# Kernel tuning notes

Hardware: AMD Instinct MI355X
Metric: run time of the kernel (lower is better)

## Reference

```python
import jax, jax.numpy as jnp
import numpy as np

# ---- ATSSPostProcessor config ----
PRE_NMS_THRESH = 0.05
PRE_NMS_TOP_N  = 400      # k candidates per image (pre_nms_top_n)
NMS_THRESH     = 0.4
POST_TOP_N     = 100      # fpn_post_nms_top_n
MIN_SIZE       = 0.0
NUM_ANGLE_BINS = 90
BBOX_W         = (10.0, 10.0, 5.0, 5.0)   # box_coder xywh weights; angle is passthrough (argmax-90 deg)
N, C, H, W     = 4, 15, 256, 256           # A=1 anchor per location
STRIDE, ANCHOR_SIZE = 8.0, 64.0
MAXV = 16                                   # vertex buffer for quad-quad clipping


def setup_inputs():
    key = jax.random.key(0)
    k1, k2, k3, k4 = jax.random.split(key, 4)
    box_cls = jax.random.normal(k1, (N, C, H, W), jnp.float32) - 2.0  # sigmoid ~0.12 avg -> plenty of candidates
    box_regression = jax.random.normal(k2, (N, 4, H, W), jnp.float32) * 0.5
    centerness = jax.random.normal(k3, (N, 1, H, W), jnp.float32)
    angle = jax.random.normal(k4, (N, NUM_ANGLE_BINS, H, W), jnp.float32)
    # xywha anchors on the stride-8 grid, row-major (H, W) to match permute_and_flatten ordering
    ys, xs = jnp.meshgrid(jnp.arange(H, dtype=jnp.float32), jnp.arange(W, dtype=jnp.float32), indexing='ij')
    cx = (xs.reshape(-1) + 0.5) * STRIDE
    cy = (ys.reshape(-1) + 0.5) * STRIDE
    wh = jnp.full((H * W,), ANCHOR_SIZE, jnp.float32)
    a0 = jnp.zeros((H * W,), jnp.float32)
    anchors = jnp.broadcast_to(jnp.stack([cx, cy, wh, wh, a0], -1), (N, H * W, 5))
    return {"box_cls": box_cls, "box_regression": box_regression, "centerness": centerness,
            "angle": angle, "anchors": jnp.asarray(anchors)}


def xywha_to_corners(b):
    # b [..., 5] (cx,cy,w,h,angle_deg) -> [..., 4, 2], CCW order
    cx, cy, w, h, a = b[..., 0], b[..., 1], b[..., 2], b[..., 3], b[..., 4]
    t = a * (jnp.pi / 180.0)
    c, s = jnp.cos(t), jnp.sin(t)
    ox = jnp.asarray([1., -1., -1., 1.], b.dtype) * (w[..., None] * 0.5)
    oy = jnp.asarray([1., 1., -1., -1.], b.dtype) * (h[..., None] * 0.5)
    x = cx[..., None] + ox * c[..., None] - oy * s[..., None]
    y = cy[..., None] + ox * s[..., None] + oy * c[..., None]
    return jnp.stack([x, y], -1)


def _clip_edge(poly, n, p1, p2):
    # Sutherland-Hodgman: clip CCW polygon (poly[:n]) against half-plane left of p1->p2
    e = p2 - p1
    d = e[0] * (poly[:, 1] - p1[1]) - e[1] * (poly[:, 0] - p1[0])  # >= 0 is inside
    def body(i, carry):
        out, m = carry
        j = jnp.where(i == n - 1, 0, i + 1)
        cur, nxt, dc, dn = poly[i], poly[j], d[i], d[j]
        denom = dc - dn
        denom = jnp.where(jnp.abs(denom) < 1e-8, 1e-8, denom)
        ip = cur + (dc / denom) * (nxt - cur)
        act = i < n
        a1 = act & (dc >= 0)
        out = out.at[m].set(jnp.where(a1, cur, out[m]))
        m = m + a1.astype(jnp.int32)
        a2 = act & ((dc >= 0) != (dn >= 0))
        out = out.at[m].set(jnp.where(a2, ip, out[m]))
        m = m + a2.astype(jnp.int32)
        return out, m
    return jax.lax.fori_loop(0, 8, body, (jnp.zeros_like(poly), jnp.int32(0)))


def _quad_inter_area(c1, c2):
    # intersection area of two CCW quads via polygon clipping + shoelace
    poly = jnp.zeros((MAXV, 2), c1.dtype).at[:4].set(c1)
    n = jnp.int32(4)
    def edge(e, carry):
        poly, n = carry
        return _clip_edge(poly, n, c2[e], c2[(e + 1) % 4])
    poly, n = jax.lax.fori_loop(0, 4, edge, (poly, n))
    idx = jnp.arange(MAXV)
    j = jnp.where(idx == n - 1, 0, idx + 1)
    mask = idx < n
    terms = poly[:, 0] * poly[j, 1] - poly[j, 0] * poly[:, 1]
    return 0.5 * jnp.abs(jnp.sum(jnp.where(mask, terms, 0.0)))


def _riou_matrix(boxes):                        # [k,5] -> [k,k] rotated IoU
    corners = xywha_to_corners(boxes)           # [k,4,2]
    areas = boxes[:, 2] * boxes[:, 3]
    def one(ci, ai):
        def two(cj, aj):
            inter = _quad_inter_area(ci, cj)
            return inter / (ai + aj - inter + 1e-7)
        return jax.vmap(two)(corners, areas)
    return jax.vmap(one)(corners, areas)


@jax.jit
def _forward(box_cls, box_regression, centerness, angle, anchors):
    n, c, h, w = box_cls.shape
    K, k = h * w, PRE_NMS_TOP_N
    # permute_and_flatten + activations
    cls = jax.nn.sigmoid(box_cls).transpose(0, 2, 3, 1).reshape(n, K, c)
    reg = box_regression.transpose(0, 2, 3, 1).reshape(n, K, 4)
    ctr = jax.nn.sigmoid(centerness).reshape(n, K)
    ang = jax.nn.softmax(angle.transpose(0, 2, 3, 1).reshape(n, K, NUM_ANGLE_BINS), axis=-1)
    # pre-nms threshold on raw sigmoid cls, topk on cls*centerness
    cand = cls > PRE_NMS_THRESH
    comb = cls * ctr[:, :, None]
    flat = jnp.where(cand, comb, -1.0).reshape(n, K * c)
    topv, topi = jax.lax.top_k(flat, k)          # sorted descending
    valid = topv > 0.0                           # emulates per_pre_nms_top_n clamp
    loc = topi // c
    labels = topi % c + 1
    reg_s = jnp.take_along_axis(reg, loc[..., None], axis=1)       # [n,k,4]
    anc_s = jnp.take_along_axis(anchors, loc[..., None], axis=1)   # [n,k,5]
    ang_s = jnp.take_along_axis(ang, loc[..., None], axis=1)       # [n,k,90]
    pred_angle = jnp.argmax(ang_s, axis=-1).astype(reg_s.dtype) - 90.0
    # box_coder.decode (xywh deltas, angle passthrough)
    wx, wy, ww, wh = BBOX_W
    dx, dy = reg_s[..., 0] / wx, reg_s[..., 1] / wy
    dw = jnp.clip(reg_s[..., 2] / ww, -10.0, 4.0)
    dh = jnp.clip(reg_s[..., 3] / wh, -10.0, 4.0)
    acx, acy, aw, ah = anc_s[..., 0], anc_s[..., 1], anc_s[..., 2], anc_s[..., 3]
    boxes = jnp.stack([dx * aw + acx, dy * ah + acy,
                       aw * jnp.exp(dw), ah * jnp.exp(dh), pred_angle], -1)
    valid = valid & (boxes[..., 2] >= MIN_SIZE) & (boxes[..., 3] >= MIN_SIZE)
    scores = jnp.where(valid, jnp.sqrt(jnp.maximum(topv, 0.0)), 0.0)
    # class-aware rotated NMS (boxlist_ml_rnms): IoU only within same class
    iou = jax.lax.stop_gradient(jax.vmap(_riou_matrix)(boxes))     # [n,k,k]
    same = labels[:, :, None] == labels[:, None, :]
    iou = jnp.where(same, iou, 0.0)
    idxs = jnp.arange(k)
    def body(i, keep):
        sup = keep[:, i][:, None] & (iou[:, i, :] > NMS_THRESH) & (idxs[None, :] > i)
        return keep & ~sup
    keep = jax.lax.fori_loop(0, k, body, valid)
    # keep top fpn_post_nms_top_n by score
    fscore = jnp.where(keep, scores, -1.0)
    fv, fi = jax.lax.top_k(fscore, POST_TOP_N)
    fvalid = fv > 0.0
    fboxes = jnp.take_along_axis(boxes, fi[..., None], axis=1)
    flabels = jnp.take_along_axis(labels, fi, axis=1)
    corners = xywha_to_corners(fboxes).reshape(n, POST_TOP_N, 8)   # convert('xyxyxyxy')
    out = jnp.concatenate([corners,
                           jnp.maximum(fv, 0.0)[..., None],
                           flabels.astype(corners.dtype)[..., None],
                           fvalid.astype(corners.dtype)[..., None]], -1)
    return out * fvalid[..., None].astype(out.dtype)   # [N, POST_TOP_N, 11]


def reference(box_cls, box_regression, centerness, angle, anchors):
    return _forward(box_cls, box_regression, centerness, angle, anchors)
```

## Files before the change

### kernel.cpp

```cpp
#include <hip/hip_runtime.h>
#include <math.h>

#define NIMG 4
#define NCLS 15
#define HW 65536
#define NANG 90
#define KTOP 400
#define POSTN 100
#define NBINS 4096
#define CAP 4096

#define HIST_OFF   0
#define CNT_OFF    65536
#define SUPT_OFF   65600
#define ZERO_BYTES 165952
#define CAND_OFF   165952
#define SKEY_OFF   297024
#define COR_OFF    309824
#define AREA_OFF   361024
#define LAB_OFF    367424
#define SC_OFF     373824
#define VAL_OFF    380224
#define CCX_OFF    386624
#define CCY_OFF    393024
#define CRAD_OFF   399424

__device__ __forceinline__ float sigmoidf(float x) {
    return 1.0f / (1.0f + expf(-x));
}

__global__ __launch_bounds__(256)
void k_hist(const float* __restrict__ cls, const float* __restrict__ ctr,
            int* __restrict__ hist) {
    __shared__ int sh[NBINS];
    const int n = blockIdx.y;
    const int p4 = (blockIdx.x * 256 + threadIdx.x) * 4;
    for (int b = threadIdx.x; b < NBINS; b += 256) sh[b] = 0;
    __syncthreads();
    float4 cv4 = *(const float4*)(ctr + n * HW + p4);
    float cv[4] = {sigmoidf(cv4.x), sigmoidf(cv4.y), sigmoidf(cv4.z), sigmoidf(cv4.w)};
    for (int j = 0; j < NCLS; ++j) {
        float4 s4 = *(const float4*)(cls + (size_t)(n * NCLS + j) * HW + p4);
        float sv[4] = {s4.x, s4.y, s4.z, s4.w};
#pragma unroll
        for (int e = 0; e < 4; ++e) {
            float s = sigmoidf(sv[e]);
            if (s > 0.05f) {
                float comb = s * cv[e];
                int b = (int)(comb * 4096.0f);
                b = b < 0 ? 0 : (b > NBINS - 1 ? NBINS - 1 : b);
                atomicAdd(&sh[b], 1);
            }
        }
    }
    __syncthreads();
    for (int b = threadIdx.x; b < NBINS; b += 256) {
        int v = sh[b];
        if (v) atomicAdd(&hist[n * NBINS + b], v);
    }
}

__global__ __launch_bounds__(256)
void k_collect(const float* __restrict__ cls, const float* __restrict__ ctr,
               const int* __restrict__ hist, int* __restrict__ cnt,
               unsigned long long* __restrict__ cand) {
    const int n = blockIdx.y;
    __shared__ int part[256];
    __shared__ int s_t;
    {
        const int* hb = hist + n * NBINS;
        int s = 0;
        int base = threadIdx.x * 16;
        for (int b = 0; b < 16; ++b) s += hb[base + b];
        part[threadIdx.x] = s;
        __syncthreads();
        if (threadIdx.x == 0) {
            int acc = 0, seg = -1, above = 0;
            for (int sg = 255; sg >= 0; --sg) {
                int ps = part[sg];
                if (acc + ps >= KTOP) { seg = sg; above = acc; break; }
                acc += ps;
            }
            int t = 0;
            if (seg >= 0) {
                int a2 = above;
                t = seg * 16;
                for (int b = seg * 16 + 15; b >= seg * 16; --b) {
                    a2 += hb[b];
                    if (a2 >= KTOP) { t = b; break; }
                }
            }
            s_t = t;
        }
        __syncthreads();
    }
    const int t = s_t;
    const int p4 = (blockIdx.x * 256 + threadIdx.x) * 4;
    float4 cv4 = *(const float4*)(ctr + n * HW + p4);
    float cv[4] = {sigmoidf(cv4.x), sigmoidf(cv4.y), sigmoidf(cv4.z), sigmoidf(cv4.w)};
    for (int j = 0; j < NCLS; ++j) {
        float4 s4 = *(const float4*)(cls + (size_t)(n * NCLS + j) * HW + p4);
        float sv[4] = {s4.x, s4.y, s4.z, s4.w};
#pragma unroll
        for (int e = 0; e < 4; ++e) {
            float s = sigmoidf(sv[e]);
            if (s > 0.05f) {
                float comb = s * cv[e];
                int b = (int)(comb * 4096.0f);
                b = b < 0 ? 0 : (b > NBINS - 1 ? NBINS - 1 : b);
                if (b >= t) {
                    int pos = atomicAdd(&cnt[n], 1);
                    if (pos < CAP) {
                        unsigned int fb  = __float_as_uint(comb);
                        unsigned int idx = (unsigned int)((p4 + e) * NCLS + j);
                        cand[n * CAP + pos] =
                            ((unsigned long long)fb << 32) | (unsigned long long)(~idx);
                    }
                }
            }
        }
    }
}

__global__ __launch_bounds__(256)
void k_select(const unsigned long long* __restrict__ cand, const int* __restrict__ cnt,
              unsigned long long* __restrict__ skey) {
    const int n = blockIdx.x;
    __shared__ unsigned long long key[CAP];
    int c = cnt[n];
    if (c > CAP) c = CAP;
    int S = 512;
    while (S < c) S <<= 1;
    for (int t = threadIdx.x; t < S; t += 256)
        key[t] = (t < c) ? cand[n * CAP + t] : 0ULL;
    __syncthreads();
    for (int k = 2; k <= S; k <<= 1) {
        for (int j = k >> 1; j > 0; j >>= 1) {
            for (int i = threadIdx.x; i < S; i += 256) {
                int l = i ^ j;
                if (l > i) {
                    unsigned long long a = key[i], b = key[l];
                    bool up = ((i & k) == 0);
                    if ((a > b) == up) { key[i] = b; key[l] = a; }
                }
            }
            __syncthreads();
        }
    }
    for (int r = threadIdx.x; r < KTOP; r += 256)
        skey[n * KTOP + r] = key[S - 1 - r];
}

__global__ __launch_bounds__(64)
void k_decode(const unsigned long long* __restrict__ skey,
              const float* __restrict__ reg, const float* __restrict__ ang,
              const float* __restrict__ anchors,
              float* __restrict__ cor, float* __restrict__ area, int* __restrict__ lab,
              float* __restrict__ sc, int* __restrict__ val,
              float* __restrict__ ccx, float* __restrict__ ccy, float* __restrict__ crad) {
#pragma clang fp contract(off)
    const int r = blockIdx.x;
    const int n = blockIdx.y;
    const int l = threadIdx.x;
    const int base = n * KTOP + r;
    unsigned long long kk = skey[base];
    if (kk == 0ULL) {
        if (l == 0) {
            val[base] = 0; sc[base] = 0.0f; lab[base] = 0; area[base] = 0.0f;
            ccx[base] = 0.0f; ccy[base] = 0.0f; crad[base] = 0.0f;
            for (int q = 0; q < 8; ++q) cor[base * 8 + q] = 0.0f;
        }
        return;
    }
    unsigned int idx = ~((unsigned int)kk);
    int loc = (int)(idx / 15u);
    const float* ap = ang + ((size_t)n * NANG) * HW + loc;
    float bv = -INFINITY; int bb = 1000;
    for (int b = l; b < NANG; b += 64) {
        float v = ap[(size_t)b * HW];
        if (v > bv) { bv = v; bb = b; }
    }
    for (int off = 32; off > 0; off >>= 1) {
        float ov = __shfl_down(bv, off);
        int   ob = __shfl_down(bb, off);
        if (ov > bv || (ov == bv && ob < bb)) { bv = ov; bb = ob; }
    }
    if (l == 0) {
        int cl = (int)(idx % 15u);
        float topv = __uint_as_float((unsigned int)(kk >> 32));
        const float* rp = reg + ((size_t)n * 4) * HW + loc;
        float dx = rp[0] / 10.0f;
        float dy = rp[HW] / 10.0f;
        float dw = rp[2 * (size_t)HW] / 5.0f;
        float dh = rp[3 * (size_t)HW] / 5.0f;
        dw = fminf(fmaxf(dw, -10.0f), 4.0f);
        dh = fminf(fmaxf(dh, -10.0f), 4.0f);
        const float* an = anchors + ((size_t)n * HW + loc) * 5;
        float acx = an[0], acy = an[1], aw = an[2], ah = an[3];
        float bcx = dx * aw + acx;
        float bcy = dy * ah + acy;
        float bw = aw * expf(dw);
        float bh = ah * expf(dh);
        float pa = (float)bb - 90.0f;
        float th = pa * (float)0.017453292519943295;
        float cth = cosf(th), sth = sinf(th);
        float hw2 = bw * 0.5f, hh2 = bh * 0.5f;
        const float oxs[4] = {1.0f, -1.0f, -1.0f, 1.0f};
        const float oys[4] = {1.0f, 1.0f, -1.0f, -1.0f};
        for (int q = 0; q < 4; ++q) {
            float ox = oxs[q] * hw2, oy = oys[q] * hh2;
            cor[base * 8 + 2 * q]     = bcx + ox * cth - oy * sth;
            cor[base * 8 + 2 * q + 1] = bcy + ox * sth + oy * cth;
        }
        val[base] = 1;
        sc[base] = sqrtf(topv);
        lab[base] = cl + 1;
        area[base] = bw * bh;
        ccx[base] = bcx; ccy[base] = bcy;
        crad[base] = 0.5f * sqrtf(bw * bw + bh * bh);
    }
}

__device__ __forceinline__ float arr_get8(const float* a, int idx) {
    float r = a[0];
#pragma unroll
    for (int s = 1; s < 8; ++s) r = (s == idx) ? a[s] : r;
    return r;
}
__device__ __forceinline__ void arr_set8(float* a, int idx, float v) {
#pragma unroll
    for (int s = 0; s < 8; ++s) a[s] = (s == idx) ? v : a[s];
}

__device__ float quad_inter_area(const float* c1x, const float* c1y,
                                 const float* c2x, const float* c2y) {
#pragma clang fp contract(off)
    float px[8], py[8], qx[8], qy[8];
    int n = 4;
#pragma unroll
    for (int i = 0; i < 8; ++i) { px[i] = (i < 4) ? c1x[i] : 0.0f;
                                  py[i] = (i < 4) ? c1y[i] : 0.0f;
                                  qx[i] = 0.0f; qy[i] = 0.0f; }
#pragma unroll
    for (int e = 0; e < 4; ++e) {
        float p1x = c2x[e], p1y = c2y[e];
        int e2 = (e + 1) & 3;
        float ex = c2x[e2] - p1x, ey = c2y[e2] - p1y;
        int m = 0;
#pragma unroll
        for (int i = 0; i < 8; ++i) {
            if (i < n) {
                int j = (i == n - 1) ? 0 : i + 1;
                float cxi = px[i], cyi = py[i];
                float cxj = arr_get8(px, j), cyj = arr_get8(py, j);
                float dc = ex * (cyi - p1y) - ey * (cxi - p1x);
                float dn = ex * (cyj - p1y) - ey * (cxj - p1x);
                bool ic = (dc >= 0.0f), in2 = (dn >= 0.0f);
                if (ic) { arr_set8(qx, m, cxi); arr_set8(qy, m, cyi); ++m; }
                if (ic != in2) {
                    float denom = dc - dn;
                    if (fabsf(denom) < 1e-8f) denom = 1e-8f;
                    float tp = dc / denom;
                    arr_set8(qx, m, cxi + tp * (cxj - cxi));
                    arr_set8(qy, m, cyi + tp * (cyj - cyi));
                    ++m;
                }
            }
        }
        n = m;
        if (n == 0) return 0.0f;
#pragma unroll
        for (int i = 0; i < 8; ++i) { px[i] = qx[i]; py[i] = qy[i]; }
    }
    float ssum = 0.0f;
#pragma unroll
    for (int i = 0; i < 8; ++i) {
        if (i < n) {
            int j = (i == n - 1) ? 0 : i + 1;
            ssum += px[i] * arr_get8(py, j) - arr_get8(px, j) * py[i];
        }
    }
    return 0.5f * fabsf(ssum);
}

__global__ __launch_bounds__(256)
void k_pairs(const float* __restrict__ cor, const float* __restrict__ area,
             const int* __restrict__ lab,
             const float* __restrict__ ccx, const float* __restrict__ ccy,
             const float* __restrict__ crad,
             unsigned long long* __restrict__ supT) {
#pragma clang fp contract(off)
    const int n = blockIdx.y;
    const int p = blockIdx.x * 256 + threadIdx.x;
    if (p >= KTOP * KTOP) return;
    const int i = p / KTOP;
    const int j = p - i * KTOP;
    if (j <= i) return;
    const int base = n * KTOP;
    const int li = lab[base + i];
    if (li == 0 || lab[base + j] != li) return;
    float dx = ccx[base + i] - ccx[base + j];
    float dy = ccy[base + i] - ccy[base + j];
    float rr = crad[base + i] + crad[base + j];
    if (dx * dx + dy * dy > rr * rr) return;
    float cix[4], ciy[4], cjx[4], cjy[4];
    for (int q = 0; q < 4; ++q) {
        cix[q] = cor[(base + i) * 8 + 2 * q]; ciy[q] = cor[(base + i) * 8 + 2 * q + 1];
        cjx[q] = cor[(base + j) * 8 + 2 * q]; cjy[q] = cor[(base + j) * 8 + 2 * q + 1];
    }
    float inter = quad_inter_area(cix, ciy, cjx, cjy);
    float iou = inter / (area[base + i] + area[base + j] - inter + 1e-7f);
    if (iou > 0.4f) {
        atomicOr(&supT[((size_t)(n * 7 + (j >> 6)) * 7 + (i >> 6)) * 64 + (j & 63)],
                 1ULL << (i & 63));
    }
}

__global__ __launch_bounds__(64)
void k_nms_out(const unsigned long long* __restrict__ supT,
               const int* __restrict__ val,
               const float* __restrict__ cor, const float* __restrict__ sc,
               const int* __restrict__ lab, float* __restrict__ out) {
    const int n = blockIdx.x;
    const int l = threadIdx.x;
    unsigned removed = 0;
#pragma unroll
    for (int t = 0; t < 7; ++t) {
        int r = 64 * t + l;
        int v = (r < KTOP) ? val[n * KTOP + r] : 0;
        if (!v) removed |= (1u << t);
    }
    unsigned long long cm[7][7];
#pragma unroll
    for (int t = 0; t < 7; ++t)
#pragma unroll
        for (int rb = 0; rb < 7; ++rb)
            cm[t][rb] = supT[((size_t)(n * 7 + t) * 7 + rb) * 64 + l];
#pragma unroll
    for (int rb = 0; rb < 7; ++rb) {
        const int lim = (rb == 6) ? (KTOP - 384) : 64;
        for (int ib = 0; ib < lim; ++ib) {
            unsigned rm = (unsigned)__builtin_amdgcn_readlane((int)removed, ib);
            if (!((rm >> rb) & 1u)) {
                removed |= ((unsigned)((cm[0][rb] >> ib) & 1ULL));
                removed |= ((unsigned)((cm[1][rb] >> ib) & 1ULL)) << 1;
                removed |= ((unsigned)((cm[2][rb] >> ib) & 1ULL)) << 2;
                removed |= ((unsigned)((cm[3][rb] >> ib) & 1ULL)) << 3;
                removed |= ((unsigned)((cm[4][rb] >> ib) & 1ULL)) << 4;
                removed |= ((unsigned)((cm[5][rb] >> ib) & 1ULL)) << 5;
                removed |= ((unsigned)((cm[6][rb] >> ib) & 1ULL)) << 6;
            }
        }
    }
    __shared__ int order[POSTN];
    int rank = 0;
#pragma unroll
    for (int t = 0; t < 7; ++t) {
        bool kb = !((removed >> t) & 1u) && (64 * t + l < KTOP);
        unsigned long long m = __ballot(kb);
        int my = rank + __popcll(m & ((1ULL << l) - 1ULL));
        if (kb && my < POSTN) order[my] = 64 * t + l;
        rank += __popcll(m);
    }
    int kcnt = rank < POSTN ? rank : POSTN;
    __syncthreads();
    for (int e = l; e < POSTN * 11; e += 64) {
        int r = e / 11, c = e - r * 11;
        float v = 0.0f;
        if (r < kcnt) {
            int i = order[r];
            int b = n * KTOP + i;
            if (c < 8)       v = cor[b * 8 + c];
            else if (c == 8) v = sc[b];
            else if (c == 9) v = (float)lab[b];
            else             v = 1.0f;
        }
        out[(n * POSTN + r) * 11 + c] = v;
    }
}

extern "C" void kernel_launch(void* const* d_in, const int* in_sizes, int n_in,
                              void* d_out, int out_size, void* d_ws, size_t ws_size,
                              hipStream_t stream) {
    const float* box_cls = (const float*)d_in[0];
    const float* box_reg = (const float*)d_in[1];
    const float* ctr     = (const float*)d_in[2];
    const float* ang     = (const float*)d_in[3];
    const float* anchors = (const float*)d_in[4];
    float* out = (float*)d_out;
    char* ws = (char*)d_ws;

    int* hist = (int*)(ws + HIST_OFF);
    int* cnt  = (int*)(ws + CNT_OFF);
    unsigned long long* supT = (unsigned long long*)(ws + SUPT_OFF);
    unsigned long long* cand = (unsigned long long*)(ws + CAND_OFF);
    unsigned long long* skey = (unsigned long long*)(ws + SKEY_OFF);
    float* cor  = (float*)(ws + COR_OFF);
    float* area = (float*)(ws + AREA_OFF);
    int* lab    = (int*)(ws + LAB_OFF);
    float* sc   = (float*)(ws + SC_OFF);
    int* val    = (int*)(ws + VAL_OFF);
    float* ccx  = (float*)(ws + CCX_OFF);
    float* ccy  = (float*)(ws + CCY_OFF);
    float* crad = (float*)(ws + CRAD_OFF);

    hipMemsetAsync(d_ws, 0, ZERO_BYTES, stream);
    k_hist   <<<dim3(HW / 1024, NIMG), 256, 0, stream>>>(box_cls, ctr, hist);
    k_collect<<<dim3(HW / 1024, NIMG), 256, 0, stream>>>(box_cls, ctr, hist, cnt, cand);
    k_select <<<NIMG, 256, 0, stream>>>(cand, cnt, skey);
    k_decode <<<dim3(KTOP, NIMG), 64, 0, stream>>>(skey, box_reg, ang, anchors,
                                                   cor, area, lab, sc, val, ccx, ccy, crad);
    k_pairs  <<<dim3((KTOP * KTOP + 255) / 256, NIMG), 256, 0, stream>>>(
                 cor, area, lab, ccx, ccy, crad, supT);
    k_nms_out<<<NIMG, 64, 0, stream>>>(supT, val, cor, sc, lab, out);
}
```

Before: 256.9 us.

## Fuse select, decode, pairwise IoU and NMS into one per-image kernel

Replaces the four tail kernels (sort, decode, pairwise IoU, NMS/output) with a single 1024-thread block per image that keeps all intermediates in shared memory. The suppression bitmask moves from global 64-bit atomics to shared 32-bit atomics that reuse the sort buffer. The aim is to cut kernel launch overhead and global round trips for small intermediates, and to shrink the memset. The cost is that the 160k-pair IoU work now runs on only 4 blocks instead of roughly 2500, which may serialise that stage heavily.

```diff
diff --git a/kernel.cpp b/kernel.cpp
--- a/kernel.cpp
+++ b/kernel.cpp
@@ -12,18 +12,8 @@
 
 #define HIST_OFF   0
 #define CNT_OFF    65536
-#define SUPT_OFF   65600
-#define ZERO_BYTES 165952
-#define CAND_OFF   165952
-#define SKEY_OFF   297024
-#define COR_OFF    309824
-#define AREA_OFF   361024
-#define LAB_OFF    367424
-#define SC_OFF     373824
-#define VAL_OFF    380224
-#define CCX_OFF    386624
-#define CCY_OFF    393024
-#define CRAD_OFF   399424
+#define ZERO_BYTES 65600
+#define CAND_OFF   65600
 
 __device__ __forceinline__ float sigmoidf(float x) {
     return 1.0f / (1.0f + expf(-x));
@@ -122,105 +112,6 @@
     }
 }
 
-__global__ __launch_bounds__(256)
-void k_select(const unsigned long long* __restrict__ cand, const int* __restrict__ cnt,
-              unsigned long long* __restrict__ skey) {
-    const int n = blockIdx.x;
-    __shared__ unsigned long long key[CAP];
-    int c = cnt[n];
-    if (c > CAP) c = CAP;
-    int S = 512;
-    while (S < c) S <<= 1;
-    for (int t = threadIdx.x; t < S; t += 256)
-        key[t] = (t < c) ? cand[n * CAP + t] : 0ULL;
-    __syncthreads();
-    for (int k = 2; k <= S; k <<= 1) {
-        for (int j = k >> 1; j > 0; j >>= 1) {
-            for (int i = threadIdx.x; i < S; i += 256) {
-                int l = i ^ j;
-                if (l > i) {
-                    unsigned long long a = key[i], b = key[l];
-                    bool up = ((i & k) == 0);
-                    if ((a > b) == up) { key[i] = b; key[l] = a; }
-                }
-            }
-            __syncthreads();
-        }
-    }
-    for (int r = threadIdx.x; r < KTOP; r += 256)
-        skey[n * KTOP + r] = key[S - 1 - r];
-}
-
-__global__ __launch_bounds__(64)
-void k_decode(const unsigned long long* __restrict__ skey,
-              const float* __restrict__ reg, const float* __restrict__ ang,
-              const float* __restrict__ anchors,
-              float* __restrict__ cor, float* __restrict__ area, int* __restrict__ lab,
-              float* __restrict__ sc, int* __restrict__ val,
-              float* __restrict__ ccx, float* __restrict__ ccy, float* __restrict__ crad) {
-#pragma clang fp contract(off)
-    const int r = blockIdx.x;
-    const int n = blockIdx.y;
-    const int l = threadIdx.x;
-    const int base = n * KTOP + r;
-    unsigned long long kk = skey[base];
-    if (kk == 0ULL) {
-        if (l == 0) {
-            val[base] = 0; sc[base] = 0.0f; lab[base] = 0; area[base] = 0.0f;
-            ccx[base] = 0.0f; ccy[base] = 0.0f; crad[base] = 0.0f;
-            for (int q = 0; q < 8; ++q) cor[base * 8 + q] = 0.0f;
-        }
-        return;
-    }
-    unsigned int idx = ~((unsigned int)kk);
-    int loc = (int)(idx / 15u);
-    const float* ap = ang + ((size_t)n * NANG) * HW + loc;
-    float bv = -INFINITY; int bb = 1000;
-    for (int b = l; b < NANG; b += 64) {
-        float v = ap[(size_t)b * HW];
-        if (v > bv) { bv = v; bb = b; }
-    }
-    for (int off = 32; off > 0; off >>= 1) {
-        float ov = __shfl_down(bv, off);
-        int   ob = __shfl_down(bb, off);
-        if (ov > bv || (ov == bv && ob < bb)) { bv = ov; bb = ob; }
-    }
-    if (l == 0) {
-        int cl = (int)(idx % 15u);
-        float topv = __uint_as_float((unsigned int)(kk >> 32));
-        const float* rp = reg + ((size_t)n * 4) * HW + loc;
-        float dx = rp[0] / 10.0f;
-        float dy = rp[HW] / 10.0f;
-        float dw = rp[2 * (size_t)HW] / 5.0f;
-        float dh = rp[3 * (size_t)HW] / 5.0f;
-        dw = fminf(fmaxf(dw, -10.0f), 4.0f);
-        dh = fminf(fmaxf(dh, -10.0f), 4.0f);
-        const float* an = anchors + ((size_t)n * HW + loc) * 5;
-        float acx = an[0], acy = an[1], aw = an[2], ah = an[3];
-        float bcx = dx * aw + acx;
-        float bcy = dy * ah + acy;
-        float bw = aw * expf(dw);
-        float bh = ah * expf(dh);
-        float pa = (float)bb - 90.0f;
-        float th = pa * (float)0.017453292519943295;
-        float cth = cosf(th), sth = sinf(th);
-        float hw2 = bw * 0.5f, hh2 = bh * 0.5f;
-        const float oxs[4] = {1.0f, -1.0f, -1.0f, 1.0f};
-        const float oys[4] = {1.0f, 1.0f, -1.0f, -1.0f};
-        for (int q = 0; q < 4; ++q) {
-            float ox = oxs[q] * hw2, oy = oys[q] * hh2;
-            cor[base * 8 + 2 * q]     = bcx + ox * cth - oy * sth;
-            cor[base * 8 + 2 * q + 1] = bcy + ox * sth + oy * cth;
-        }
-        val[base] = 1;
-        sc[base] = sqrtf(topv);
-        lab[base] = cl + 1;
-        area[base] = bw * bh;
-        ccx[base] = bcx; ccy[base] = bcy;
-        crad[base] = 0.5f * sqrtf(bw * bw + bh * bh);
-    }
-}
-
 __device__ __forceinline__ float arr_get8(const float* a, int idx) {
     float r = a[0];
 #pragma unroll
@@ -283,99 +174,190 @@
     return 0.5f * fabsf(ssum);
 }
 
-__global__ __launch_bounds__(256)
-void k_pairs(const float* __restrict__ cor, const float* __restrict__ area,
-             const int* __restrict__ lab,
-             const float* __restrict__ ccx, const float* __restrict__ ccy,
-             const float* __restrict__ crad,
-             unsigned long long* __restrict__ supT) {
+__global__ __launch_bounds__(1024)
+void k_tail(const unsigned long long* __restrict__ cand, const int* __restrict__ cnt,
+            const float* __restrict__ reg, const float* __restrict__ ang,
+            const float* __restrict__ anchors, float* __restrict__ out) {
 #pragma clang fp contract(off)
-    const int n = blockIdx.y;
-    const int p = blockIdx.x * 256 + threadIdx.x;
-    if (p >= KTOP * KTOP) return;
-    const int i = p / KTOP;
-    const int j = p - i * KTOP;
-    if (j <= i) return;
-    const int base = n * KTOP;
-    const int li = lab[base + i];
-    if (li == 0 || lab[base + j] != li) return;
-    float dx = ccx[base + i] - ccx[base + j];
-    float dy = ccy[base + i] - ccy[base + j];
-    float rr = crad[base + i] + crad[base + j];
-    if (dx * dx + dy * dy > rr * rr) return;
-    float cix[4], ciy[4], cjx[4], cjy[4];
-    for (int q = 0; q < 4; ++q) {
-        cix[q] = cor[(base + i) * 8 + 2 * q]; ciy[q] = cor[(base + i) * 8 + 2 * q + 1];
-        cjx[q] = cor[(base + j) * 8 + 2 * q]; cjy[q] = cor[(base + j) * 8 + 2 * q + 1];
-    }
-    float inter = quad_inter_area(cix, ciy, cjx, cjy);
-    float iou = inter / (area[base + i] + area[base + j] - inter + 1e-7f);
-    if (iou > 0.4f) {
-        atomicOr(&supT[((size_t)(n * 7 + (j >> 6)) * 7 + (i >> 6)) * 64 + (j & 63)],
-                 1ULL << (i & 63));
-    }
-}
-
-__global__ __launch_bounds__(64)
-void k_nms_out(const unsigned long long* __restrict__ supT,
-               const int* __restrict__ val,
-               const float* __restrict__ cor, const float* __restrict__ sc,
-               const int* __restrict__ lab, float* __restrict__ out) {
     const int n = blockIdx.x;
-    const int l = threadIdx.x;
-    unsigned removed = 0;
-#pragma unroll
-    for (int t = 0; t < 7; ++t) {
-        int r = 64 * t + l;
-        int v = (r < KTOP) ? val[n * KTOP + r] : 0;
-        if (!v) removed |= (1u << t);
-    }
-    unsigned long long cm[7][7];
-#pragma unroll
-    for (int t = 0; t < 7; ++t)
-#pragma unroll
-        for (int rb = 0; rb < 7; ++rb)
-            cm[t][rb] = supT[((size_t)(n * 7 + t) * 7 + rb) * 64 + l];
-#pragma unroll
-    for (int rb = 0; rb < 7; ++rb) {
-        const int lim = (rb == 6) ? (KTOP - 384) : 64;
-        for (int ib = 0; ib < lim; ++ib) {
-            unsigned rm = (unsigned)__builtin_amdgcn_readlane((int)removed, ib);
-            if (!((rm >> rb) & 1u)) {
-                removed |= ((unsigned)((cm[0][rb] >> ib) & 1ULL));
-                removed |= ((unsigned)((cm[1][rb] >> ib) & 1ULL)) << 1;
-                removed |= ((unsigned)((cm[2][rb] >> ib) & 1ULL)) << 2;
-                removed |= ((unsigned)((cm[3][rb] >> ib) & 1ULL)) << 3;
-                removed |= ((unsigned)((cm[4][rb] >> ib) & 1ULL)) << 4;
-                removed |= ((unsigned)((cm[5][rb] >> ib) & 1ULL)) << 5;
-                removed |= ((unsigned)((cm[6][rb] >> ib) & 1ULL)) << 6;
-            }
-        }
-    }
-    __shared__ int order[POSTN];
-    int rank = 0;
-#pragma unroll
-    for (int t = 0; t < 7; ++t) {
-        bool kb = !((removed >> t) & 1u) && (64 * t + l < KTOP);
-        unsigned long long m = __ballot(kb);
-        int my = rank + __popcll(m & ((1ULL << l) - 1ULL));
-        if (kb && my < POSTN) order[my] = 64 * t + l;
-        rank += __popcll(m);
-    }
-    int kcnt = rank < POSTN ? rank : POSTN;
-    __syncthreads();
-    for (int e = l; e < POSTN * 11; e += 64) {
-        int r = e / 11, c = e - r * 11;
+    const int tid = threadIdx.x;
+
+    __shared__ unsigned long long keys[CAP];
+    __shared__ unsigned long long s_skey[KTOP];
+    __shared__ float s_cor[KTOP * 8];
+    __shared__ float s_cx[KTOP], s_cy[KTOP], s_rad[KTOP], s_area[KTOP], s_sc[KTOP];
+    __shared__ int   s_lab[KTOP], s_val[KTOP];
+    __shared__ int   s_order[POSTN];
+    __shared__ int   s_kcnt;
+    unsigned int* sup32 = (unsigned int*)keys;
+
+    int c = cnt[n];
+    if (c > CAP) c = CAP;
+    int S = 512;
+    while (S < c) S <<= 1;
+    for (int i = tid; i < S; i += 1024)
+        keys[i] = (i < c) ? cand[n * CAP + i] : 0ULL;
+    __syncthreads();
+    for (int k = 2; k <= S; k <<= 1) {
+        for (int j = k >> 1; j > 0; j >>= 1) {
+            for (int i = tid; i < S; i += 1024) {
+                int l = i ^ j;
+                if (l > i) {
+                    unsigned long long a = keys[i], b = keys[l];
+                    bool up = ((i & k) == 0);
+                    if ((a > b) == up) { keys[i] = b; keys[l] = a; }
+                }
+            }
+            __syncthreads();
+        }
+    }
+    for (int r = tid; r < KTOP; r += 1024)
+        s_skey[r] = keys[S - 1 - r];
+    __syncthreads();
+
+    for (int i = tid; i < 7 * 7 * 64 * 2; i += 1024) sup32[i] = 0u;
+    if (tid < 2 * KTOP) {
+        const int r = tid >> 1, half = tid & 1;
+        unsigned long long kk = s_skey[r];
+        if (kk == 0ULL) {
+            if (half == 0) {
+                s_val[r] = 0; s_sc[r] = 0.0f; s_lab[r] = 0; s_area[r] = 0.0f;
+                s_cx[r] = 0.0f; s_cy[r] = 0.0f; s_rad[r] = 0.0f;
+                for (int q = 0; q < 8; ++q) s_cor[r * 8 + q] = 0.0f;
+            }
+        } else {
+            unsigned int idx = ~((unsigned int)kk);
+            int loc = (int)(idx / 15u);
+            const float* ap = ang + ((size_t)n * NANG) * HW + loc;
+            float bv = -INFINITY; int bb = 1000;
+            for (int k2 = 0; k2 < 45; ++k2) {
+                int b = half * 45 + k2;
+                float v = ap[(size_t)b * HW];
+                if (v > bv) { bv = v; bb = b; }
+            }
+            float ov = __shfl_xor(bv, 1);
+            int   ob = __shfl_xor(bb, 1);
+            if (ov > bv || (ov == bv && ob < bb)) { bv = ov; bb = ob; }
+            if (half == 0) {
+                int cl = (int)(idx % 15u);
+                float topv = __uint_as_float((unsigned int)(kk >> 32));
+                const float* rp = reg + ((size_t)n * 4) * HW + loc;
+                float dx = rp[0] / 10.0f;
+                float dy = rp[HW] / 10.0f;
+                float dw = rp[2 * (size_t)HW] / 5.0f;
+                float dh = rp[3 * (size_t)HW] / 5.0f;
+                dw = fminf(fmaxf(dw, -10.0f), 4.0f);
+                dh = fminf(fmaxf(dh, -10.0f), 4.0f);
+                const float* an = anchors + ((size_t)n * HW + loc) * 5;
+                float acx = an[0], acy = an[1], aw = an[2], ah = an[3];
+                float bcx = dx * aw + acx;
+                float bcy = dy * ah + acy;
+                float bw = aw * expf(dw);
+                float bh = ah * expf(dh);
+                float pa = (float)bb - 90.0f;
+                float th = pa * (float)0.017453292519943295;
+                float cth = cosf(th), sth = sinf(th);
+                float hw2 = bw * 0.5f, hh2 = bh * 0.5f;
+                const float oxs[4] = {1.0f, -1.0f, -1.0f, 1.0f};
+                const float oys[4] = {1.0f, 1.0f, -1.0f, -1.0f};
+                for (int q = 0; q < 4; ++q) {
+                    float ox = oxs[q] * hw2, oy = oys[q] * hh2;
+                    s_cor[r * 8 + 2 * q]     = bcx + ox * cth - oy * sth;
+                    s_cor[r * 8 + 2 * q + 1] = bcy + ox * sth + oy * cth;
+                }
+                s_val[r] = 1;
+                s_sc[r] = sqrtf(topv);
+                s_lab[r] = cl + 1;
+                s_area[r] = bw * bh;
+                s_cx[r] = bcx; s_cy[r] = bcy;
+                s_rad[r] = 0.5f * sqrtf(bw * bw + bh * bh);
+            }
+        }
+    }
+    __syncthreads();
+
+    for (int p = tid; p < KTOP * KTOP; p += 1024) {
+        int i = p / KTOP;
+        int j = p - i * KTOP;
+        if (j <= i) continue;
+        int li = s_lab[i];
+        if (li == 0 || s_lab[j] != li) continue;
+        float dx = s_cx[i] - s_cx[j], dy = s_cy[i] - s_cy[j];
+        float rr = s_rad[i] + s_rad[j];
+        if (dx * dx + dy * dy > rr * rr) continue;
+        float cix[4], ciy[4], cjx[4], cjy[4];
+        for (int q = 0; q < 4; ++q) {
+            cix[q] = s_cor[i * 8 + 2 * q]; ciy[q] = s_cor[i * 8 + 2 * q + 1];
+            cjx[q] = s_cor[j * 8 + 2 * q]; cjy[q] = s_cor[j * 8 + 2 * q + 1];
+        }
+        float inter = quad_inter_area(cix, ciy, cjx, cjy);
+        float iou = inter / (s_area[i] + s_area[j] - inter + 1e-7f);
+        if (iou > 0.4f) {
+            int base = (((j >> 6) * 7 + (i >> 6)) * 64 + (j & 63)) * 2 + ((i >> 5) & 1);
+            atomicOr(&sup32[base], 1u << (i & 31));
+        }
+    }
+    __syncthreads();
+
+    if (tid < 64) {
+        const int l = tid;
+        unsigned removed = 0;
+#pragma unroll
+        for (int t = 0; t < 7; ++t) {
+            int r = 64 * t + l;
+            int v = (r < KTOP) ? s_val[r] : 0;
+            if (!v) removed |= (1u << t);
+        }
+        unsigned long long cm[7][7];
+#pragma unroll
+        for (int t = 0; t < 7; ++t)
+#pragma unroll
+            for (int rb = 0; rb < 7; ++rb) {
+                int bi = ((t * 7 + rb) * 64 + l) * 2;
+                cm[t][rb] = (unsigned long long)sup32[bi] |
+                            ((unsigned long long)sup32[bi + 1] << 32);
+            }
+#pragma unroll
+        for (int rb = 0; rb < 7; ++rb) {
+            const int lim = (rb == 6) ? (KTOP - 384) : 64;
+            for (int ib = 0; ib < lim; ++ib) {
+                unsigned rm = (unsigned)__builtin_amdgcn_readlane((int)removed, ib);
+                if (!((rm >> rb) & 1u)) {
+                    removed |= ((unsigned)((cm[0][rb] >> ib) & 1ULL));
+                    removed |= ((unsigned)((cm[1][rb] >> ib) & 1ULL)) << 1;
+                    removed |= ((unsigned)((cm[2][rb] >> ib) & 1ULL)) << 2;
+                    removed |= ((unsigned)((cm[3][rb] >> ib) & 1ULL)) << 3;
+                    removed |= ((unsigned)((cm[4][rb] >> ib) & 1ULL)) << 4;
+                    removed |= ((unsigned)((cm[5][rb] >> ib) & 1ULL)) << 5;
+                    removed |= ((unsigned)((cm[6][rb] >> ib) & 1ULL)) << 6;
+                }
+            }
+        }
+        int rank = 0;
+#pragma unroll
+        for (int t = 0; t < 7; ++t) {
+            bool kb = !((removed >> t) & 1u) && (64 * t + l < KTOP);
+            unsigned long long m = __ballot(kb);
+            int my = rank + __popcll(m & ((1ULL << l) - 1ULL));
+            if (kb && my < POSTN) s_order[my] = 64 * t + l;
+            rank += __popcll(m);
+        }
+        if (l == 0) s_kcnt = (rank < POSTN) ? rank : POSTN;
+    }
+    __syncthreads();
+
+    const int kcnt = s_kcnt;
+    for (int e = tid; e < POSTN * 11; e += 1024) {
+        int r = e / 11, col = e - r * 11;
         float v = 0.0f;
         if (r < kcnt) {
-            int i = order[r];
-            int b = n * KTOP + i;
-            if (c < 8)       v = cor[b * 8 + c];
-            else if (c == 8) v = sc[b];
-            else if (c == 9) v = (float)lab[b];
-            else             v = 1.0f;
-        }
-        out[(n * POSTN + r) * 11 + c] = v;
+            int i = s_order[r];
+            if (col < 8)        v = s_cor[i * 8 + col];
+            else if (col == 8)  v = s_sc[i];
+            else if (col == 9)  v = (float)s_lab[i];
+            else                v = 1.0f;
+        }
+        out[(n * POSTN + r) * 11 + col] = v;
     }
 }
 
@@ -392,25 +374,10 @@
 
     int* hist = (int*)(ws + HIST_OFF);
     int* cnt  = (int*)(ws + CNT_OFF);
-    unsigned long long* supT = (unsigned long long*)(ws + SUPT_OFF);
     unsigned long long* cand = (unsigned long long*)(ws + CAND_OFF);
-    unsigned long long* skey = (unsigned long long*)(ws + SKEY_OFF);
-    float* cor  = (float*)(ws + COR_OFF);
-    float* area = (float*)(ws + AREA_OFF);
-    int* lab    = (int*)(ws + LAB_OFF);
-    float* sc   = (float*)(ws + SC_OFF);
-    int* val    = (int*)(ws + VAL_OFF);
-    float* ccx  = (float*)(ws + CCX_OFF);
-    float* ccy  = (float*)(ws + CCY_OFF);
-    float* crad = (float*)(ws + CRAD_OFF);
 
     hipMemsetAsync(d_ws, 0, ZERO_BYTES, stream);
     k_hist   <<<dim3(HW / 1024, NIMG), 256, 0, stream>>>(box_cls, ctr, hist);
     k_collect<<<dim3(HW / 1024, NIMG), 256, 0, stream>>>(box_cls, ctr, hist, cnt, cand);
-    k_select <<<NIMG, 256, 0, stream>>>(cand, cnt, skey);
-    k_decode <<<dim3(KTOP, NIMG), 64, 0, stream>>>(skey, box_reg, ang, anchors,
-                                                   cor, area, lab, sc, val, ccx, ccy, crad);
-    k_pairs  <<<dim3((KTOP * KTOP + 255) / 256, NIMG), 256, 0, stream>>>(
-                 cor, area, lab, ccx, ccy, crad, supT);
-    k_nms_out<<<NIMG, 64, 0, stream>>>(supT, val, cor, sc, lab, out);
-}
+    k_tail   <<<NIMG, 1024, 0, stream>>>(cand, cnt, box_reg, ang, anchors, out);
+}
```

Result: slower. 348.0 us (+35.5%).
